# Performance work log

Hardware: AMD Instinct MI355X
Metric: run time of the kernel (lower is better)

Reference implementation:

```python
import jax, jax.numpy as jnp
import numpy as np

B, S, D, H, R, N, KR = 2, 2048, 1024, 16, 256, 8, 128
DH = D // H
EPS = 1e-5


def setup_inputs() -> dict:
    key = jax.random.key(0)
    ks = jax.random.split(key, 20)
    sm = lambda k, n: jax.nn.softmax(jax.random.normal(k, (B, S, n), jnp.float32), axis=-1)
    return {
        "x": jax.random.normal(ks[0], (B, S, D), jnp.float32),
        "fqk_w_Q": sm(ks[1], N),
        "fqk_w_K": sm(ks[2], N),
        "fv_w": sm(ks[3], N),
        "rqk_w_Q": sm(ks[4], N),
        "rqk_w_K": sm(ks[5], N),
        "rv_w": sm(ks[6], N),
        "feature_know_w": sm(ks[7], N),
        "restore_know_w": sm(ks[8], N),
        "f_qk": jax.random.normal(ks[9], (N, D, R), jnp.float32) * 0.02,
        "f_v": jax.random.normal(ks[10], (N, D, R), jnp.float32) * 0.02,
        "r_qk": jax.random.normal(ks[11], (N, R, D), jnp.float32) * 0.02,
        "r_v": jax.random.normal(ks[12], (N, R, D), jnp.float32) * 0.02,
        "f_know": jax.random.normal(ks[13], (N, D, KR), jnp.float32) * 0.02,
        "r_know": jax.random.normal(ks[14], (N, KR, D), jnp.float32) * 0.02,
        "W_O": jax.random.normal(ks[15], (D, D), jnp.float32) * 0.02,
        "ln1_g": jnp.ones((D,), jnp.float32),
        "ln1_b": jnp.zeros((D,), jnp.float32),
        "ln2_g": jnp.ones((D,), jnp.float32),
        "ln2_b": jnp.zeros((D,), jnp.float32),
    }


def _layernorm(x, g, b):
    m = jnp.mean(x, axis=-1, keepdims=True)
    v = jnp.mean(jnp.square(x - m), axis=-1, keepdims=True)
    return (x - m) * jax.lax.rsqrt(v + EPS) * g + b


def _feature(x, neurons, w):
    # fused form of einsum('bsd,ndr->bsnr') + einsum('bsnr,bsn->bsr')
    return jnp.einsum('bsd,bsn,ndr->bsr', x, w, neurons)


def _restore(h, neurons, w):
    # fused form of einsum('bsr,nrd->bsnd') + einsum('bsnd,bsn->bsd')
    return jnp.einsum('bsr,bsn,nrd->bsd', h, w, neurons)


def _causal_sdpa(q, k, v):
    # q,k,v: [B,H,S,DH]
    scores = jnp.einsum('bhqd,bhkd->bhqk', q, k) / jnp.sqrt(jnp.float32(DH))
    mask = jnp.tril(jnp.ones((S, S), bool))
    scores = jnp.where(mask, scores, jnp.finfo(scores.dtype).min)
    p = jax.nn.softmax(scores, axis=-1)
    return jnp.einsum('bhqk,bhkd->bhqd', p, v)


def _block(x, fqk_w_Q, fqk_w_K, fv_w, rqk_w_Q, rqk_w_K, rv_w,
           feature_know_w, restore_know_w, f_qk, f_v, r_qk, r_v,
           f_know, r_know, W_O, ln1_g, ln1_b, ln2_g, ln2_b):
    nx = _layernorm(x, ln1_g, ln1_b)
    h_q = _feature(nx, f_qk, fqk_w_Q)
    h_k = _feature(nx, f_qk, fqk_w_K)
    h_v = _feature(nx, f_v, fv_w)
    Q = _restore(h_q, r_qk, rqk_w_Q)
    K = _restore(h_k, r_qk, rqk_w_K)
    V = _restore(h_v, r_v, rv_w)
    to_heads = lambda t: t.reshape(B, S, H, DH).transpose(0, 2, 1, 3)
    attn = _causal_sdpa(to_heads(Q), to_heads(K), to_heads(V))
    attn = attn.transpose(0, 2, 1, 3).reshape(B, S, D)
    attn_out = attn @ W_O.T  # nn.Linear(d_model,d_model,bias=False)
    x = x + attn_out
    nx2 = _layernorm(x, ln2_g, ln2_b)
    h = _feature(nx2, f_know, feature_know_w)
    know_out = _restore(h, r_know, restore_know_w)
    return x + know_out


def reference(x, fqk_w_Q, fqk_w_K, fv_w, rqk_w_Q, rqk_w_K, rv_w,
              feature_know_w, restore_know_w, f_qk, f_v, r_qk, r_v,
              f_know, r_know, W_O, ln1_g, ln1_b, ln2_g, ln2_b):
    return _block(x, fqk_w_Q, fqk_w_K, fv_w, rqk_w_Q, rqk_w_K, rv_w,
                  feature_know_w, restore_know_w, f_qk, f_v, r_qk, r_v,
                  f_know, r_know, W_O, ln1_g, ln1_b, ln2_g, ln2_b)
```

## Files before the change

### kernel.cpp

```cpp
#include <hip/hip_runtime.h>
#include <hip/hip_bf16.h>


typedef __bf16 bf16_t;
typedef __bf16 bf16x4 __attribute__((ext_vector_type(4)));
typedef __bf16 bf16x8 __attribute__((ext_vector_type(8)));
typedef float f32x4 __attribute__((ext_vector_type(4)));

#define B_DIM 2
#define S_LEN 2048
#define D_DIM 1024
#define H_NUM 16
#define DH 64
#define N_NEU 8
#define R_DIM 256
#define KR_DIM 128
#define ROWS (B_DIM * S_LEN)

static __device__ __forceinline__ void gl_lds16(const void* g, void* l)
{
    __builtin_amdgcn_global_load_lds(
        (__attribute__((address_space(1))) void*)(g),
        (__attribute__((address_space(3))) void*)(l), 16, 0, 0);
}

__global__ __launch_bounds__(256)
void tcast_kernel(const float* __restrict__ in, bf16_t* __restrict__ out, int I, int J)
{
    __shared__ float t[32][33];
    const int bJ = blockIdx.x * 32, bI = blockIdx.y * 32;
    const size_t boff = (size_t)blockIdx.z * I * J;
    const int tx = threadIdx.x, ty = threadIdx.y;
#pragma unroll
    for (int i = 0; i < 4; i++)
        t[ty * 4 + i][tx] = in[boff + (size_t)(bI + ty * 4 + i) * J + bJ + tx];
    __syncthreads();
#pragma unroll
    for (int i = 0; i < 4; i++)
        out[boff + (size_t)(bJ + ty * 4 + i) * I + bI + tx] = (bf16_t)t[tx][ty * 4 + i];
}

__global__ __launch_bounds__(256)
void tbf_kernel(const bf16_t* __restrict__ in, bf16_t* __restrict__ out, int I, int J)
{
    __shared__ bf16_t t[32][33];
    const int bJ = blockIdx.x * 32, bI = blockIdx.y * 32;
    const size_t boff = (size_t)blockIdx.z * I * J;
    const int tx = threadIdx.x, ty = threadIdx.y;
#pragma unroll
    for (int i = 0; i < 4; i++)
        t[ty * 4 + i][tx] = in[boff + (size_t)(bI + ty * 4 + i) * J + bJ + tx];
    __syncthreads();
#pragma unroll
    for (int i = 0; i < 4; i++)
        out[boff + (size_t)(bJ + ty * 4 + i) * I + bI + tx] = t[tx][ty * 4 + i];
}

__global__ __launch_bounds__(256)
void cast_kernel(const float* __restrict__ in, bf16_t* __restrict__ out, int n4)
{
    int i = blockIdx.x * 256 + threadIdx.x;
    if (i < n4) {
        float4 v = ((const float4*)in)[i];
        bf16_t* op = out + (size_t)i * 4;
        op[0] = (bf16_t)v.x; op[1] = (bf16_t)v.y; op[2] = (bf16_t)v.z; op[3] = (bf16_t)v.w;
    }
}

__global__ __launch_bounds__(256)
void ln_kernel(const float* __restrict__ x, const float* __restrict__ g,
               const float* __restrict__ beta, bf16_t* __restrict__ out)
{
    __shared__ float red[4];
    const int row = blockIdx.x;
    const int tid = threadIdx.x;
    float4 v = *(const float4*)&x[(size_t)row * D_DIM + tid * 4];

    float s = v.x + v.y + v.z + v.w;
#pragma unroll
    for (int o = 32; o; o >>= 1) s += __shfl_down(s, o);
    if ((tid & 63) == 0) red[tid >> 6] = s;
    __syncthreads();
    float mean = (red[0] + red[1] + red[2] + red[3]) * (1.f / D_DIM);
    __syncthreads();

    float dx = v.x - mean, dy = v.y - mean, dz = v.z - mean, dw = v.w - mean;
    float q = dx * dx + dy * dy + dz * dz + dw * dw;
#pragma unroll
    for (int o = 32; o; o >>= 1) q += __shfl_down(q, o);
    if ((tid & 63) == 0) red[tid >> 6] = q;
    __syncthreads();
    float var = (red[0] + red[1] + red[2] + red[3]) * (1.f / D_DIM);
    float rstd = rsqrtf(var + 1e-5f);

    float4 gv = *(const float4*)&g[tid * 4];
    float4 bv = *(const float4*)&beta[tid * 4];
    bf16_t* op = out + (size_t)row * D_DIM + tid * 4;
    op[0] = (bf16_t)(dx * rstd * gv.x + bv.x);
    op[1] = (bf16_t)(dy * rstd * gv.y + bv.y);
    op[2] = (bf16_t)(dz * rstd * gv.z + bv.z);
    op[3] = (bf16_t)(dw * rstd * gv.w + bv.w);
}

__global__ __launch_bounds__(256)
void ln2x_kernel(const float* __restrict__ x, const bf16_t* __restrict__ P0,
                 const bf16_t* __restrict__ P1, const float* __restrict__ g,
                 const float* __restrict__ beta, float* __restrict__ outf,
                 bf16_t* __restrict__ outn)
{
    __shared__ float red[4];
    const int row = blockIdx.x;
    const int tid = threadIdx.x;
    const size_t base = (size_t)row * D_DIM + tid * 4;
    float4 v  = *(const float4*)&x[base];
    bf16x4 p0 = *(const bf16x4*)&P0[base];
    bf16x4 p1 = *(const bf16x4*)&P1[base];
    v.x += (float)p0[0] + (float)p1[0];
    v.y += (float)p0[1] + (float)p1[1];
    v.z += (float)p0[2] + (float)p1[2];
    v.w += (float)p0[3] + (float)p1[3];
    *(float4*)&outf[base] = v;

    float s = v.x + v.y + v.z + v.w;
#pragma unroll
    for (int o = 32; o; o >>= 1) s += __shfl_down(s, o);
    if ((tid & 63) == 0) red[tid >> 6] = s;
    __syncthreads();
    float mean = (red[0] + red[1] + red[2] + red[3]) * (1.f / D_DIM);
    __syncthreads();

    float dx = v.x - mean, dy = v.y - mean, dz = v.z - mean, dw = v.w - mean;
    float q = dx * dx + dy * dy + dz * dz + dw * dw;
#pragma unroll
    for (int o = 32; o; o >>= 1) q += __shfl_down(q, o);
    if ((tid & 63) == 0) red[tid >> 6] = q;
    __syncthreads();
    float var = (red[0] + red[1] + red[2] + red[3]) * (1.f / D_DIM);
    float rstd = rsqrtf(var + 1e-5f);

    float4 gv = *(const float4*)&g[tid * 4];
    float4 bv = *(const float4*)&beta[tid * 4];
    bf16_t* op = outn + base;
    op[0] = (bf16_t)(dx * rstd * gv.x + bv.x);
    op[1] = (bf16_t)(dy * rstd * gv.y + bv.y);
    op[2] = (bf16_t)(dz * rstd * gv.z + bv.z);
    op[3] = (bf16_t)(dw * rstd * gv.w + bv.w);
}

__global__ __launch_bounds__(256)
void wsf_kernel(const bf16_t* __restrict__ y,
                const float* __restrict__ wfQ, const float* __restrict__ wrQ,
                const float* __restrict__ wfK, const float* __restrict__ wrK,
                const float* __restrict__ wfV, const float* __restrict__ wrV,
                bf16_t* __restrict__ sq, bf16_t* __restrict__ sk, bf16_t* __restrict__ sv)
{
    const int r = threadIdx.x;
    const int row = blockIdx.x;
    const bf16_t* yrow = y + (size_t)row * 4096;
    const float* fQ = wfQ + row * N_NEU;
    const float* fK = wfK + row * N_NEU;
    const float* fV = wfV + row * N_NEU;
    float aQ = 0.f, aK = 0.f, aV = 0.f;
#pragma unroll
    for (int n = 0; n < N_NEU; n++) {
        float yq = (float)yrow[n * R_DIM + r];
        float yv = (float)yrow[2048 + n * R_DIM + r];
        aQ += fQ[n] * yq;
        aK += fK[n] * yq;
        aV += fV[n] * yv;
    }
    const float* rQ = wrQ + row * N_NEU;
    const float* rK = wrK + row * N_NEU;
    const float* rV = wrV + row * N_NEU;
    const size_t rb = (size_t)row * 2048;
#pragma unroll
    for (int n = 0; n < N_NEU; n++) {
        sq[rb + n * R_DIM + r] = (bf16_t)(rQ[n] * aQ);
        sk[rb + n * R_DIM + r] = (bf16_t)(rK[n] * aK);
        sv[rb + n * R_DIM + r] = (bf16_t)(rV[n] * aV);
    }
}

__global__ __launch_bounds__(256)
void ws2_kernel(const bf16_t* __restrict__ P0, const bf16_t* __restrict__ P1,
                const float* __restrict__ wf, const float* __restrict__ wr,
                bf16_t* __restrict__ sout)
{
    const int lr = threadIdx.x >> 7;
    const int r  = threadIdx.x & 127;
    const int row = blockIdx.x * 2 + lr;
    const size_t rb = (size_t)row * (N_NEU * KR_DIM);
    const float* wfp = wf + row * N_NEU;
    const float* wrp = wr + row * N_NEU;
    float acc = 0.f;
#pragma unroll
    for (int n = 0; n < N_NEU; n++) {
        size_t i = rb + n * KR_DIM + r;
        acc += wfp[n] * ((float)P0[i] + (float)P1[i]);
    }
    bf16_t* srow = sout + rb;
#pragma unroll
    for (int n = 0; n < N_NEU; n++) srow[n * KR_DIM + r] = (bf16_t)(wrp[n] * acc);
}

template<int EPI>
__global__ __launch_bounds__(256)
void gemm_kernel(const bf16_t* __restrict__ A, const bf16_t* __restrict__ Bt,
                 const bf16_t* __restrict__ Bt2, int splitMy,
                 void* Cout, const float* resid, int M, int N, int K)
{
    __shared__ bf16_t As[3][128][32];
    __shared__ bf16_t Bs[3][128][32];
    const int tid = threadIdx.x;
    const int l = tid & 63, w = tid >> 6;
    const int wr = w >> 1, wc = w & 1;

    const int nbxy = gridDim.x * gridDim.y;
    int bid = blockIdx.y * gridDim.x + blockIdx.x;
    if ((nbxy & 7) == 0) bid = (bid & 7) * (nbxy >> 3) + (bid >> 3);
    const int bx = bid % gridDim.x, by = bid / gridDim.x;

    const int m0 = by * 128, n0 = bx * 128;
    const bf16_t* Bsel = (by < splitMy) ? Bt : Bt2;

    int kbeg = 0, kend = K;
    if constexpr (EPI == 2) { const int half = K >> 1; kbeg = blockIdx.z * half; kend = kbeg + half; }

    const int srow = l >> 2;
    const int scolswz = (((l & 3) * 16) ^ ((srow & 6) << 3)) >> 1;
    const bf16_t* Ag0 = A    + (size_t)(m0 + w * 32 + srow) * K + scolswz;
    const bf16_t* Ag1 = Ag0 + (size_t)16 * K;
    const bf16_t* Bg0 = Bsel + (size_t)(n0 + w * 32 + srow) * K + scolswz;
    const bf16_t* Bg1 = Bg0 + (size_t)16 * K;

    auto stage = [&](int buf, int k0) {
        char* Asb = (char*)&As[buf][0][0] + w * 2048;
        char* Bsb = (char*)&Bs[buf][0][0] + w * 2048;
        gl_lds16(Ag0 + k0, Asb);
        gl_lds16(Ag1 + k0, Asb + 1024);
        gl_lds16(Bg0 + k0, Bsb);
        gl_lds16(Bg1 + k0, Bsb + 1024);
    };

    f32x4 acc[4][4];
    const f32x4 zero = {0.f, 0.f, 0.f, 0.f};
#pragma unroll
    for (int i = 0; i < 4; i++)
#pragma unroll
        for (int j = 0; j < 4; j++) acc[i][j] = zero;

    const int fr = l & 15;
    const int fkb = (l >> 4) * 16;

    stage(0, kbeg);
    stage(1, kbeg + 32);

    const int nK = (kend - kbeg) >> 5;
    for (int it = 0; it < nK; ++it) {
        if (it + 1 < nK) {
            asm volatile("s_waitcnt vmcnt(4)" ::: "memory");
        } else {
            asm volatile("s_waitcnt vmcnt(0)" ::: "memory");
        }
        __builtin_amdgcn_s_barrier();
        __builtin_amdgcn_sched_barrier(0);

        const int cur = it % 3;
        const char* Ab = (const char*)&As[cur][0][0];
        const char* Bb = (const char*)&Bs[cur][0][0];
        bf16x8 af[4], bv[4];
#pragma unroll
        for (int i = 0; i < 4; i++) {
            const int rowA = wr * 64 + i * 16 + fr;
            af[i] = *(const bf16x8*)(Ab + rowA * 64 + (fkb ^ ((rowA & 6) << 3)));
        }
#pragma unroll
        for (int i = 0; i < 4; i++) {
            const int rowB = wc * 64 + i * 16 + fr;
            bv[i] = *(const bf16x8*)(Bb + rowB * 64 + (fkb ^ ((rowB & 6) << 3)));
        }

        if (it + 2 < nK) stage((it + 2) % 3, kbeg + (it + 2) * 32);

        __builtin_amdgcn_s_setprio(1);
#pragma unroll
        for (int mi = 0; mi < 4; mi++)
#pragma unroll
            for (int ni = 0; ni < 4; ni++)
                acc[mi][ni] = __builtin_amdgcn_mfma_f32_16x16x32_bf16(af[mi], bv[ni], acc[mi][ni], 0, 0, 0);
        __builtin_amdgcn_s_setprio(0);
    }

    const int orow = (l >> 4) * 4;
    const int ocol = l & 15;
#pragma unroll
    for (int mi = 0; mi < 4; mi++)
#pragma unroll
        for (int ni = 0; ni < 4; ni++)
#pragma unroll
            for (int j = 0; j < 4; j++) {
                int row = m0 + wr * 64 + mi * 16 + orow + j;
                int col = n0 + wc * 64 + ni * 16 + ocol;
                size_t idx = (size_t)row * N + col;
                if constexpr (EPI == 0) {
                    ((bf16_t*)Cout)[idx] = (bf16_t)acc[mi][ni][j];
                } else if constexpr (EPI == 1) {
                    ((float*)Cout)[idx] = acc[mi][ni][j] + resid[idx];
                } else {
                    ((bf16_t*)Cout)[(size_t)blockIdx.z * M * N + idx] = (bf16_t)acc[mi][ni][j];
                }
            }
}

__global__ __launch_bounds__(256)
void fa_kernel(const bf16_t* __restrict__ Q, const bf16_t* __restrict__ K,
               const bf16_t* __restrict__ Vt, bf16_t* __restrict__ O)
{
    __shared__ bf16_t Ks[128][72];
    __shared__ bf16_t Vs[64][136];
    __shared__ bf16_t Ps[4][16][136];

    const int tid = threadIdx.x;
    const int l = tid & 63, w = tid >> 6;

    const int bid  = blockIdx.x;
    const int xcd  = bid & 7;
    const int slot = bid >> 3;
    const int head = slot & 3;
    const int jq   = slot >> 2;
    const int bh   = xcd * 4 + head;
    const int b = bh >> 4, h = bh & 15;

    const bf16_t* Qp = Q + (size_t)b * S_LEN * D_DIM + h * DH;
    const bf16_t* Kp = K + (size_t)b * S_LEN * D_DIM + h * DH;
    const bf16_t* Vp = Vt + (size_t)b * D_DIM * S_LEN + (size_t)h * DH * S_LEN;

    const int fr = l & 15, fg = l >> 4, fk = fg * 8;
    const int srow = tid >> 2;
    const int scol = (tid & 3) * 16;
    const bf16_t* Kst = Kp + (size_t)srow * D_DIM + scol;
    const bf16_t* Vst = Vp + (size_t)srow * S_LEN + scol;

    bf16x8 ones8;
#pragma unroll
    for (int i = 0; i < 8; i++) ones8[i] = (bf16_t)1.f;

    const f32x4 zero = {0.f, 0.f, 0.f, 0.f};
    const float C_LOG2 = 0.125f * 1.44269504f;

    for (int pass = 0; pass < 2; ++pass) {
        const int qb = pass ? jq : (31 - jq);
        const int q0 = qb * 64;
        const int nt = (qb >> 1) + 1;

        bf16x8 qf[2];
#pragma unroll
        for (int ks = 0; ks < 2; ks++)
            qf[ks] = *(const bf16x8*)(Qp + (size_t)(q0 + w * 16 + fr) * D_DIM + ks * 32 + fk);

        f32x4 o[4];
        f32x4 la = zero;
        float m_r[4];
#pragma unroll
        for (int j = 0; j < 4; j++) { o[j] = zero; m_r[j] = -1e30f; }

        uint4 kva = *(const uint4*)(Kst);
        uint4 kvb = *(const uint4*)(Kst + 8);
        uint4 kvc = *(const uint4*)(Kst + (size_t)64 * D_DIM);
        uint4 kvd = *(const uint4*)(Kst + (size_t)64 * D_DIM + 8);
        uint4 vva = *(const uint4*)(Vst);
        uint4 vvb = *(const uint4*)(Vst + 8);
        uint4 vvc = *(const uint4*)(Vst + 64);
        uint4 vvd = *(const uint4*)(Vst + 72);

        for (int t = 0; t < nt; t++) {
            const int k0 = t * 128;
            __syncthreads();
            *(uint4*)&Ks[srow][scol]          = kva;
            *(uint4*)&Ks[srow][scol + 8]      = kvb;
            *(uint4*)&Ks[64 + srow][scol]     = kvc;
            *(uint4*)&Ks[64 + srow][scol + 8] = kvd;
            *(uint4*)&Vs[srow][scol]          = vva;
            *(uint4*)&Vs[srow][scol + 8]      = vvb;
            *(uint4*)&Vs[srow][64 + scol]     = vvc;
            *(uint4*)&Vs[srow][64 + scol + 8] = vvd;
            __syncthreads();

            if (t + 1 < nt) {
                const int kn = k0 + 128;
                kva = *(const uint4*)(Kst + (size_t)kn * D_DIM);
                kvb = *(const uint4*)(Kst + (size_t)kn * D_DIM + 8);
                kvc = *(const uint4*)(Kst + (size_t)(kn + 64) * D_DIM);
                kvd = *(const uint4*)(Kst + (size_t)(kn + 64) * D_DIM + 8);
                vva = *(const uint4*)(Vst + kn);
                vvb = *(const uint4*)(Vst + kn + 8);
                vvc = *(const uint4*)(Vst + kn + 64);
                vvd = *(const uint4*)(Vst + kn + 72);
            }

            f32x4 sc[2][4];
#pragma unroll
            for (int s2 = 0; s2 < 2; s2++)
#pragma unroll
                for (int ni = 0; ni < 4; ni++) sc[s2][ni] = zero;
            __builtin_amdgcn_s_setprio(1);
#pragma unroll
            for (int ks = 0; ks < 2; ks++) {
#pragma unroll
                for (int s2 = 0; s2 < 2; s2++)
#pragma unroll
                    for (int ni = 0; ni < 4; ni++) {
                        bf16x8 kf = *(const bf16x8*)&Ks[s2 * 64 + ni * 16 + fr][ks * 32 + fk];
                        sc[s2][ni] = __builtin_amdgcn_mfma_f32_16x16x32_bf16(qf[ks], kf, sc[s2][ni], 0, 0, 0);
                    }
            }
            __builtin_amdgcn_s_setprio(0);

            float p[2][4][4];
            if (t == nt - 1) {
#pragma unroll
                for (int s2 = 0; s2 < 2; s2++)
#pragma unroll
                    for (int ni = 0; ni < 4; ni++) {
                        const int key = k0 + s2 * 64 + ni * 16 + fr;
#pragma unroll
                        for (int j = 0; j < 4; j++) {
                            const int qg = q0 + w * 16 + fg * 4 + j;
                            p[s2][ni][j] = (key <= qg) ? sc[s2][ni][j] * C_LOG2 : -1e30f;
                        }
                    }
            } else {
#pragma unroll
                for (int s2 = 0; s2 < 2; s2++)
#pragma unroll
                    for (int ni = 0; ni < 4; ni++)
#pragma unroll
                        for (int j = 0; j < 4; j++)
                            p[s2][ni][j] = sc[s2][ni][j] * C_LOG2;
            }

#pragma unroll
            for (int j = 0; j < 4; j++) {
                float rmax = p[0][0][j];
#pragma unroll
                for (int s2 = 0; s2 < 2; s2++)
#pragma unroll
                    for (int ni = 0; ni < 4; ni++) rmax = fmaxf(rmax, p[s2][ni][j]);
#pragma unroll
                for (int d = 1; d < 16; d <<= 1) rmax = fmaxf(rmax, __shfl_xor(rmax, d));
                if (rmax > m_r[j] + 8.f) {
                    float scale = exp2f(m_r[j] - rmax);
                    la[j] *= scale;
#pragma unroll
                    for (int nc = 0; nc < 4; nc++) o[nc][j] *= scale;
                    m_r[j] = rmax;
                }
#pragma unroll
                for (int s2 = 0; s2 < 2; s2++)
#pragma unroll
                    for (int ni = 0; ni < 4; ni++)
                        p[s2][ni][j] = exp2f(p[s2][ni][j] - m_r[j]);
            }

#pragma unroll
            for (int s2 = 0; s2 < 2; s2++)
#pragma unroll
                for (int ni = 0; ni < 4; ni++)
#pragma unroll
                    for (int j = 0; j < 4; j++)
                        Ps[w][fg * 4 + j][s2 * 64 + ni * 16 + fr] = (bf16_t)p[s2][ni][j];

            __builtin_amdgcn_s_setprio(1);
#pragma unroll
            for (int ks = 0; ks < 4; ks++) {
                bf16x8 pa = *(const bf16x8*)&Ps[w][fr][ks * 32 + fk];
                la = __builtin_amdgcn_mfma_f32_16x16x32_bf16(pa, ones8, la, 0, 0, 0);
#pragma unroll
                for (int nc = 0; nc < 4; nc++) {
                    bf16x8 vf = *(const bf16x8*)&Vs[nc * 16 + fr][ks * 32 + fk];
                    o[nc] = __builtin_amdgcn_mfma_f32_16x16x32_bf16(pa, vf, o[nc], 0, 0, 0);
                }
            }
            __builtin_amdgcn_s_setprio(0);
        }

#pragma unroll
        for (int j = 0; j < 4; j++) {
            const float inv = 1.f / la[j];
            const int q = q0 + w * 16 + fg * 4 + j;
            bf16_t* op = O + (size_t)(b * S_LEN + q) * D_DIM + h * DH;
#pragma unroll
            for (int nc = 0; nc < 4; nc++)
                op[nc * 16 + fr] = (bf16_t)(o[nc][j] * inv);
        }
    }
}

extern "C" void kernel_launch(void* const* d_in, const int* in_sizes, int n_in,
                              void* d_out, int out_size, void* d_ws, size_t ws_size,
                              hipStream_t stream)
{
    const float* x      = (const float*)d_in[0];
    const float* fqk_wQ = (const float*)d_in[1];
    const float* fqk_wK = (const float*)d_in[2];
    const float* fv_w   = (const float*)d_in[3];
    const float* rqk_wQ = (const float*)d_in[4];
    const float* rqk_wK = (const float*)d_in[5];
    const float* rv_w   = (const float*)d_in[6];
    const float* fkn_w  = (const float*)d_in[7];
    const float* rkn_w  = (const float*)d_in[8];
    const float* f_qk   = (const float*)d_in[9];
    const float* f_v    = (const float*)d_in[10];
    const float* r_qk   = (const float*)d_in[11];
    const float* r_v    = (const float*)d_in[12];
    const float* f_know = (const float*)d_in[13];
    const float* r_know = (const float*)d_in[14];
    const float* W_O    = (const float*)d_in[15];
    const float* ln1g   = (const float*)d_in[16];
    const float* ln1b   = (const float*)d_in[17];
    const float* ln2g   = (const float*)d_in[18];
    const float* ln2b   = (const float*)d_in[19];
    float* out_f = (float*)d_out;
    (void)ws_size; (void)in_sizes; (void)n_in; (void)out_size;

    char* ws = (char*)d_ws;
    const size_t MB = 1024 * 1024;
    bf16_t* rqkT   = (bf16_t*)(ws + 0 * MB);
    bf16_t* rvT    = (bf16_t*)(ws + 4 * MB);
    bf16_t* rknT   = (bf16_t*)(ws + 8 * MB);
    bf16_t* woB    = (bf16_t*)(ws + 10 * MB);
    bf16_t* fknT   = (bf16_t*)(ws + 12 * MB);
    bf16_t* buf_nx = (bf16_t*)(ws + 14 * MB);
    bf16_t* buf_y  = (bf16_t*)(ws + 22 * MB);
    char*   buf_s  = ws + 54 * MB;
    bf16_t* fqkT   = (bf16_t*)(buf_s);
    bf16_t* fvT    = (bf16_t*)(buf_s + 4 * MB);
    bf16_t* s_q    = (bf16_t*)(buf_s);
    bf16_t* s_k    = (bf16_t*)(buf_s) + (size_t)4096 * 2048;
    bf16_t* s_v    = (bf16_t*)(buf_s) + (size_t)8192 * 2048;
    bf16_t* attn   = (bf16_t*)(buf_s);
    bf16_t* P0     = (bf16_t*)(buf_s + 16 * MB);
    bf16_t* P0k    = (bf16_t*)(buf_s);
    bf16_t* sk2    = (bf16_t*)(buf_s + 32 * MB);
    bf16_t* Qb     = buf_y;
    bf16_t* Kb     = buf_y + (size_t)4096 * 1024;
    bf16_t* Vb     = buf_y + (size_t)8192 * 1024;
    bf16_t* Vt     = buf_nx;

    const dim3 blk256(256), blkT(32, 8);

    tcast_kernel<<<dim3(R_DIM / 32, D_DIM / 32, N_NEU), blkT, 0, stream>>>(f_qk, fqkT, D_DIM, R_DIM);
    tcast_kernel<<<dim3(R_DIM / 32, D_DIM / 32, N_NEU), blkT, 0, stream>>>(f_v, fvT, D_DIM, R_DIM);
    tcast_kernel<<<dim3(KR_DIM / 32, D_DIM / 32, N_NEU), blkT, 0, stream>>>(f_know, fknT, D_DIM, KR_DIM);
    tcast_kernel<<<dim3(D_DIM / 32, 2048 / 32, 1), blkT, 0, stream>>>(r_qk, rqkT, 2048, D_DIM);
    tcast_kernel<<<dim3(D_DIM / 32, 2048 / 32, 1), blkT, 0, stream>>>(r_v, rvT, 2048, D_DIM);
    tcast_kernel<<<dim3(D_DIM / 32, 1024 / 32, 1), blkT, 0, stream>>>(r_know, rknT, 1024, D_DIM);
    cast_kernel<<<dim3(1024 * 1024 / 4 / 256), blk256, 0, stream>>>(W_O, woB, 1024 * 1024 / 4);

    ln_kernel<<<dim3(ROWS), blk256, 0, stream>>>(x, ln1g, ln1b, buf_nx);

    gemm_kernel<0><<<dim3(32, 32), blk256, 0, stream>>>(buf_nx, fqkT, fqkT, 1 << 30, buf_y, nullptr, 4096, 4096, 1024);

    wsf_kernel<<<dim3(ROWS), blk256, 0, stream>>>(buf_y, fqk_wQ, rqk_wQ, fqk_wK, rqk_wK, fv_w, rv_w, s_q, s_k, s_v);

    gemm_kernel<0><<<dim3(8, 96), blk256, 0, stream>>>((bf16_t*)buf_s, rqkT, rvT, 64, buf_y, nullptr, 12288, 1024, 2048);

    tbf_kernel<<<dim3(D_DIM / 32, S_LEN / 32, B_DIM), blkT, 0, stream>>>(Vb, Vt, S_LEN, D_DIM);

    fa_kernel<<<dim3(512), blk256, 0, stream>>>(Qb, Kb, Vt, attn);

    gemm_kernel<2><<<dim3(8, 32, 2), blk256, 0, stream>>>(attn, woB, woB, 1 << 30, P0, nullptr, 4096, 1024, 1024);

    ln2x_kernel<<<dim3(ROWS), blk256, 0, stream>>>(x, P0, P0 + (size_t)4096 * 1024, ln2g, ln2b, out_f, buf_nx);

    gemm_kernel<2><<<dim3(8, 32, 2), blk256, 0, stream>>>(buf_nx, fknT, fknT, 1 << 30, P0k, nullptr, 4096, 1024, 1024);

    ws2_kernel<<<dim3(ROWS / 2), blk256, 0, stream>>>(P0k, P0k + (size_t)4096 * 1024, fkn_w, rkn_w, sk2);

    gemm_kernel<1><<<dim3(8, 32), blk256, 0, stream>>>(sk2, rknT, rknT, 1 << 30, d_out, out_f, 4096, 1024, 1024);
}
```

Baseline: 302.0 us.

## Add 256x128 tile GEMM with 8 warps for bf16-output GEMMs

Adds a gemm256 kernel using 512 threads and a 256x128 output tile. It keeps the triple-buffered global_load_lds pipeline but splits each k-step into two MFMA halves, interleaving the A and B prefetches between them. Four of the five GEMMs move to this kernel to raise B-tile reuse and cut global traffic per FLOP. The grids halve, so SM fill drops for the smaller GEMMs, and the larger tile adds LDS and register pressure. The old kernel is reduced to the residual fp32 epilogue only.

```diff
diff --git a/kernel.cpp b/kernel.cpp
--- a/kernel.cpp
+++ b/kernel.cpp
@@ -204,6 +204,130 @@
 }
 
 template<int EPI>
+__global__ __launch_bounds__(512, 2)
+void gemm256_kernel(const bf16_t* __restrict__ A, const bf16_t* __restrict__ Bt,
+                    const bf16_t* __restrict__ Bt2, int splitMy,
+                    void* Cout, int M, int N, int K)
+{
+    __shared__ bf16_t As[3][256][32];
+    __shared__ bf16_t Bs[3][128][32];
+    const int tid = threadIdx.x;
+    const int l = tid & 63, w = tid >> 6;
+    const int wr = w >> 1, wc = w & 1;
+
+    const int nbxy = gridDim.x * gridDim.y;
+    int bid = blockIdx.y * gridDim.x + blockIdx.x;
+    if ((nbxy & 7) == 0) bid = (bid & 7) * (nbxy >> 3) + (bid >> 3);
+    const int bx = bid % gridDim.x, by = bid / gridDim.x;
+
+    const int m0 = by * 256, n0 = bx * 128;
+    const bf16_t* Bsel = (by < splitMy) ? Bt : Bt2;
+
+    int kbeg = 0, kend = K;
+    if constexpr (EPI == 2) { const int half = K >> 1; kbeg = blockIdx.z * half; kend = kbeg + half; }
+
+    const int strow  = w * 16 + (l >> 2);
+    const int scelem = ((((l & 3) * 16) ^ ((strow & 6) << 3)) >> 1);
+    const bf16_t* Ag0 = A    + (size_t)(m0 + strow) * K + scelem;
+    const bf16_t* Ag1 = A    + (size_t)(m0 + strow + 128) * K + scelem;
+    const bf16_t* Bg0 = Bsel + (size_t)(n0 + strow) * K + scelem;
+
+    auto stageA = [&](int buf, int k0) {
+        char* d = (char*)&As[buf][0][0] + w * 1024;
+        gl_lds16(Ag0 + k0, d);
+        gl_lds16(Ag1 + k0, d + 8192);
+    };
+    auto stageB = [&](int buf, int k0) {
+        char* d = (char*)&Bs[buf][0][0] + w * 1024;
+        gl_lds16(Bg0 + k0, d);
+    };
+
+    f32x4 acc[4][4];
+    const f32x4 zero = {0.f, 0.f, 0.f, 0.f};
+#pragma unroll
+    for (int i = 0; i < 4; i++)
+#pragma unroll
+        for (int j = 0; j < 4; j++) acc[i][j] = zero;
+
+    const int fr  = l & 15;
+    const int fkb = (l >> 4) * 16;
+
+    stageA(0, kbeg);      stageB(0, kbeg);
+    stageA(1, kbeg + 32); stageB(1, kbeg + 32);
+
+    const int nK = (kend - kbeg) >> 5;
+    for (int it = 0; it < nK; ++it) {
+        if (it + 1 < nK) {
+            asm volatile("s_waitcnt vmcnt(3)" ::: "memory");
+        } else {
+            asm volatile("s_waitcnt vmcnt(0)" ::: "memory");
+        }
+        __builtin_amdgcn_s_barrier();
+        __builtin_amdgcn_sched_barrier(0);
+
+        const int cur = it % 3;
+        const char* Ab = (const char*)&As[cur][0][0];
+        const char* Bb = (const char*)&Bs[cur][0][0];
+        const bool pf = (it + 2 < nK);
+        const int knext = kbeg + (it + 2) * 32;
+
+        if (pf) stageA((it + 2) % 3, knext);
+
+        bf16x8 bv[4], af[4];
+#pragma unroll
+        for (int i = 0; i < 4; i++) {
+            const int rowB = wc * 64 + i * 16 + fr;
+            bv[i] = *(const bf16x8*)(Bb + rowB * 64 + (fkb ^ ((rowB & 6) << 3)));
+        }
+#pragma unroll
+        for (int i = 0; i < 2; i++) {
+            const int rowA = wr * 64 + i * 16 + fr;
+            af[i] = *(const bf16x8*)(Ab + rowA * 64 + (fkb ^ ((rowA & 6) << 3)));
+        }
+        __builtin_amdgcn_s_setprio(1);
+#pragma unroll
+        for (int mi = 0; mi < 2; mi++)
+#pragma unroll
+            for (int ni = 0; ni < 4; ni++)
+                acc[mi][ni] = __builtin_amdgcn_mfma_f32_16x16x32_bf16(af[mi], bv[ni], acc[mi][ni], 0, 0, 0);
+        __builtin_amdgcn_s_setprio(0);
+        __builtin_amdgcn_s_barrier();
+
+        if (pf) stageB((it + 2) % 3, knext);
+#pragma unroll
+        for (int i = 2; i < 4; i++) {
+            const int rowA = wr * 64 + i * 16 + fr;
+            af[i] = *(const bf16x8*)(Ab + rowA * 64 + (fkb ^ ((rowA & 6) << 3)));
+        }
+        __builtin_amdgcn_s_setprio(1);
+#pragma unroll
+        for (int mi = 2; mi < 4; mi++)
+#pragma unroll
+            for (int ni = 0; ni < 4; ni++)
+                acc[mi][ni] = __builtin_amdgcn_mfma_f32_16x16x32_bf16(af[mi], bv[ni], acc[mi][ni], 0, 0, 0);
+        __builtin_amdgcn_s_setprio(0);
+    }
+
+    const int orow = (l >> 4) * 4;
+    const int ocol = l & 15;
+#pragma unroll
+    for (int mi = 0; mi < 4; mi++)
+#pragma unroll
+        for (int ni = 0; ni < 4; ni++)
+#pragma unroll
+            for (int j = 0; j < 4; j++) {
+                int row = m0 + wr * 64 + mi * 16 + orow + j;
+                int col = n0 + wc * 64 + ni * 16 + ocol;
+                size_t idx = (size_t)row * N + col;
+                if constexpr (EPI == 0) {
+                    ((bf16_t*)Cout)[idx] = (bf16_t)acc[mi][ni][j];
+                } else {
+                    ((bf16_t*)Cout)[(size_t)blockIdx.z * M * N + idx] = (bf16_t)acc[mi][ni][j];
+                }
+            }
+}
+
+template<int EPI>
 __global__ __launch_bounds__(256)
 void gemm_kernel(const bf16_t* __restrict__ A, const bf16_t* __restrict__ Bt,
                  const bf16_t* __restrict__ Bt2, int splitMy,
@@ -224,7 +348,6 @@
     const bf16_t* Bsel = (by < splitMy) ? Bt : Bt2;
 
     int kbeg = 0, kend = K;
-    if constexpr (EPI == 2) { const int half = K >> 1; kbeg = blockIdx.z * half; kend = kbeg + half; }
 
     const int srow = l >> 2;
     const int scolswz = (((l & 3) * 16) ^ ((srow & 6) << 3)) >> 1;
@@ -302,13 +425,7 @@
                 int row = m0 + wr * 64 + mi * 16 + orow + j;
                 int col = n0 + wc * 64 + ni * 16 + ocol;
                 size_t idx = (size_t)row * N + col;
-                if constexpr (EPI == 0) {
-                    ((bf16_t*)Cout)[idx] = (bf16_t)acc[mi][ni][j];
-                } else if constexpr (EPI == 1) {
-                    ((float*)Cout)[idx] = acc[mi][ni][j] + resid[idx];
-                } else {
-                    ((bf16_t*)Cout)[(size_t)blockIdx.z * M * N + idx] = (bf16_t)acc[mi][ni][j];
-                }
+                ((float*)Cout)[idx] = acc[mi][ni][j] + resid[idx];
             }
 }
 
@@ -547,7 +664,7 @@
     bf16_t* Vb     = buf_y + (size_t)8192 * 1024;
     bf16_t* Vt     = buf_nx;
 
-    const dim3 blk256(256), blkT(32, 8);
+    const dim3 blk256(256), blk512(512), blkT(32, 8);
 
     tcast_kernel<<<dim3(R_DIM / 32, D_DIM / 32, N_NEU), blkT, 0, stream>>>(f_qk, fqkT, D_DIM, R_DIM);
     tcast_kernel<<<dim3(R_DIM / 32, D_DIM / 32, N_NEU), blkT, 0, stream>>>(f_v, fvT, D_DIM, R_DIM);
@@ -559,21 +676,21 @@
 
     ln_kernel<<<dim3(ROWS), blk256, 0, stream>>>(x, ln1g, ln1b, buf_nx);
 
-    gemm_kernel<0><<<dim3(32, 32), blk256, 0, stream>>>(buf_nx, fqkT, fqkT, 1 << 30, buf_y, nullptr, 4096, 4096, 1024);
+    gemm256_kernel<0><<<dim3(32, 16), blk512, 0, stream>>>(buf_nx, fqkT, fqkT, 1 << 30, buf_y, 4096, 4096, 1024);
 
     wsf_kernel<<<dim3(ROWS), blk256, 0, stream>>>(buf_y, fqk_wQ, rqk_wQ, fqk_wK, rqk_wK, fv_w, rv_w, s_q, s_k, s_v);
 
-    gemm_kernel<0><<<dim3(8, 96), blk256, 0, stream>>>((bf16_t*)buf_s, rqkT, rvT, 64, buf_y, nullptr, 12288, 1024, 2048);
+    gemm256_kernel<0><<<dim3(8, 48), blk512, 0, stream>>>((bf16_t*)buf_s, rqkT, rvT, 32, buf_y, 12288, 1024, 2048);
 
     tbf_kernel<<<dim3(D_DIM / 32, S_LEN / 32, B_DIM), blkT, 0, stream>>>(Vb, Vt, S_LEN, D_DIM);
 
     fa_kernel<<<dim3(512), blk256, 0, stream>>>(Qb, Kb, Vt, attn);
 
-    gemm_kernel<2><<<dim3(8, 32, 2), blk256, 0, stream>>>(attn, woB, woB, 1 << 30, P0, nullptr, 4096, 1024, 1024);
+    gemm256_kernel<2><<<dim3(8, 16, 2), blk512, 0, stream>>>(attn, woB, woB, 1 << 30, P0, 4096, 1024, 1024);
 
     ln2x_kernel<<<dim3(ROWS), blk256, 0, stream>>>(x, P0, P0 + (size_t)4096 * 1024, ln2g, ln2b, out_f, buf_nx);
 
-    gemm_kernel<2><<<dim3(8, 32, 2), blk256, 0, stream>>>(buf_nx, fknT, fknT, 1 << 30, P0k, nullptr, 4096, 1024, 1024);
+    gemm256_kernel<2><<<dim3(8, 16, 2), blk512, 0, stream>>>(buf_nx, fknT, fknT, 1 << 30, P0k, 4096, 1024, 1024);
 
     ws2_kernel<<<dim3(ROWS / 2), blk256, 0, stream>>>(P0k, P0k + (size_t)4096 * 1024, fkn_w, rkn_w, sk2);
 
```

Result: slower. 316.2 us (+4.7%).
